# Performance work log

Measured on AMD Instinct MI355X. Metric: run time of the kernel, lower is better.

The kernel has to match this reference:

```python
import jax, jax.numpy as jnp
import numpy as np

HEAD = 16

def setup_inputs() -> dict:
    key = jax.random.key(0)
    k1, k2, k3 = jax.random.split(key, 3)
    B, S, D = 2, 2048, 1024
    x = jax.random.normal(k1, (B, S, D), dtype=jnp.float32)
    w_qkv = jax.random.normal(k2, (D, 3 * D), dtype=jnp.float32) * (1.0 / np.sqrt(D))
    b_qkv = jnp.zeros((3 * D,), dtype=jnp.float32)
    w_out = jax.random.normal(k3, (D, D), dtype=jnp.float32) * (1.0 / np.sqrt(D))
    b_out = jnp.zeros((D,), dtype=jnp.float32)
    return {"x": x, "w_qkv": w_qkv, "b_qkv": b_qkv, "w_out": w_out, "b_out": b_out}


def reference(x, w_qkv, b_qkv, w_out, b_out):
    B, S, D = x.shape
    hd = D // HEAD  # head dim
    qkv = x @ w_qkv + b_qkv                      # [B,S,3D]
    qkv = qkv.reshape(B, S, 3, HEAD, hd)
    qkv = jnp.transpose(qkv, (2, 0, 3, 1, 4))    # [3,B,H,S,hd]
    q, k, v = qkv[0], qkv[1], qkv[2]
    scores = jnp.einsum('bhqd,bhkd->bhqk', q, k)  # [B,H,S,S]
    causal = jnp.triu(jnp.ones((S, S), dtype=bool), k=1)
    scores = jnp.where(causal, -jnp.inf, scores)
    scores = scores / jnp.sqrt(jnp.asarray(hd, dtype=x.dtype))
    attn = jax.nn.softmax(scores, axis=-1)
    z = jnp.einsum('bhqk,bhkd->bhqd', attn, v)   # [B,H,S,hd]
    z = jnp.transpose(z, (0, 2, 1, 3)).reshape(B, S, D)
    out = z @ w_out + b_out
    return out
```

## Files before the change

### kernel.cpp

```cpp
#include <hip/hip_runtime.h>

#define S_LEN  2048
#define NH     16
#define HD     64
#define DMODEL 1024

using bf16x8 = __attribute__((ext_vector_type(8))) __bf16;
using f32x4  = __attribute__((ext_vector_type(4))) float;

__device__ __forceinline__ unsigned short f2bf(float f) {
    unsigned u = __float_as_uint(f);
    u += 0x7FFFu + ((u >> 16) & 1u);
    return (unsigned short)(u >> 16);
}
__device__ __forceinline__ unsigned pk_trunc(float lo, float hi) {
    return __builtin_amdgcn_perm(__float_as_uint(hi), __float_as_uint(lo), 0x07060302u);
}

#define EXP2(x) __builtin_amdgcn_exp2f(x)

#define GLDS16(gsrc, ldst) \
    __builtin_amdgcn_global_load_lds((__attribute__((address_space(1))) void*)(gsrc), \
                                     (__attribute__((address_space(3))) void*)(ldst), 16, 0, 0)

#define WAIT_LGKM0() __builtin_amdgcn_s_waitcnt(0xC07F)

#define ASM_VMCNT(n)  asm volatile("s_waitcnt vmcnt(" #n ")" ::: "memory")
#define ASM_BARRIER() asm volatile("s_barrier" ::: "memory")

__global__ __launch_bounds__(256) void prep_kernel(
    const float* __restrict__ x, const float* __restrict__ w_qkv,
    const float* __restrict__ w_out,
    unsigned short* __restrict__ xb, unsigned short* __restrict__ wqkvT,
    unsigned short* __restrict__ woutT) {
    __shared__ float T[32][33];
    int bx = blockIdx.x;
    if (bx < 4096) {
        int idx = (bx * 256 + threadIdx.x) * 4;
        float4 v = *(const float4*)(x + idx);
        ushort4 o;
        o.x = f2bf(v.x); o.y = f2bf(v.y); o.z = f2bf(v.z); o.w = f2bf(v.w);
        *(ushort4*)(xb + idx) = o;
        return;
    }
    int tb = bx - 4096;
    int tcol = tb & 127, krow = tb >> 7;
    const float* in;
    unsigned short* out;
    int N, nbx;
    if (tcol < 96) { in = w_qkv; out = wqkvT; N = 3072; nbx = tcol; }
    else           { in = w_out; out = woutT; N = 1024; nbx = tcol - 96; }
    int r  = threadIdx.x >> 3;
    int c4 = (threadIdx.x & 7) * 4;
    int kbase = krow * 32, nbase = nbx * 32;
    float4 v = *(const float4*)(in + (size_t)(kbase + r) * N + nbase + c4);
    T[r][c4 + 0] = v.x; T[r][c4 + 1] = v.y; T[r][c4 + 2] = v.z; T[r][c4 + 3] = v.w;
    __syncthreads();
    ushort4 o;
    o.x = f2bf(T[c4 + 0][r]); o.y = f2bf(T[c4 + 1][r]);
    o.z = f2bf(T[c4 + 2][r]); o.w = f2bf(T[c4 + 3][r]);
    *(ushort4*)(out + (size_t)(nbase + r) * 1024 + kbase + c4) = o;
}

template <int NI, int NT>
__device__ __forceinline__ void mfma_mainloop64(const unsigned short* __restrict__ A,
                                                const unsigned short* __restrict__ B,
                                                int m0, int n0,
                                                unsigned short* As, unsigned short* Bs,
                                                f32x4 acc[4][NI]) {
    constexpr int K = NT * 64;
    const int lane = threadIdx.x & 63, wave = threadIdx.x >> 6;
    const int quad = lane >> 4, l15 = lane & 15;
    const int wm0 = (wave >> 1) * 64, wn0 = (wave & 1) * (NI * 16);

    auto stageA = [&](int t) {
        unsigned short* Ad = As + (t % 3) * 8192;
        #pragma unroll
        for (int j = 0; j < 4; ++j) {
            int c0 = j * 256 + wave * 64;
            int c  = c0 + lane;
            int r = c >> 3, pc = c & 7, q = pc ^ (r & 7);
            GLDS16(A + (size_t)(m0 + r) * K + t * 64 + q * 8, Ad + c0 * 8);
        }
    };
    auto stageB = [&](int t) {
        unsigned short* Bd = Bs + (t & 1) * (NI * 2048);
        #pragma unroll
        for (int j = 0; j < NI; ++j) {
            int c0 = j * 256 + wave * 64;
            int c  = c0 + lane;
            int r = c >> 3, pc = c & 7, q = pc ^ (r & 7);
            GLDS16(B + (size_t)(n0 + r) * K + t * 64 + q * 8, Bd + c0 * 8);
        }
    };

    stageB(0); stageA(0);
    stageB(1); stageA(1);
    stageA(2);

    #pragma unroll
    for (int t = 0; t < NT; ++t) {
        if (t < NT - 1) { ASM_VMCNT(4); } else { ASM_VMCNT(0); }
        ASM_BARRIER();
        if (t >= 1) {
            if (t + 1 < NT) stageB(t + 1);
            if (t + 2 < NT) stageA(t + 2);
        }

        const unsigned short* Ab = As + (t % 3) * 8192;
        const unsigned short* Bb = Bs + (t & 1) * (NI * 2048);
        bf16x8 af[2][4], bfr[2][NI];
        #pragma unroll
        for (int mi = 0; mi < 4; ++mi) {
            int r = wm0 + mi * 16 + l15, x = r & 7;
            af[0][mi] = *(const bf16x8*)(Ab + r * 64 + ((quad    ) ^ x) * 8);
            af[1][mi] = *(const bf16x8*)(Ab + r * 64 + ((4 + quad) ^ x) * 8);
        }
        #pragma unroll
        for (int ni = 0; ni < NI; ++ni) {
            int r = wn0 + ni * 16 + l15, x = r & 7;
            bfr[0][ni] = *(const bf16x8*)(Bb + r * 64 + ((quad    ) ^ x) * 8);
            bfr[1][ni] = *(const bf16x8*)(Bb + r * 64 + ((4 + quad) ^ x) * 8);
        }
        #pragma unroll
        for (int h = 0; h < 2; ++h)
            #pragma unroll
            for (int mi = 0; mi < 4; ++mi)
                #pragma unroll
                for (int ni = 0; ni < NI; ++ni)
                    acc[mi][ni] = __builtin_amdgcn_mfma_f32_16x16x32_bf16(
                        af[h][mi], bfr[h][ni], acc[mi][ni], 0, 0, 0);
    }
}

__global__ __launch_bounds__(256) void gemm_qkv_kernel(
    const unsigned short* __restrict__ xb, const unsigned short* __restrict__ wT,
    const float* __restrict__ bias,
    unsigned short* __restrict__ Qt, unsigned short* __restrict__ Kh,
    unsigned short* __restrict__ Vt) {
    __shared__ __align__(16) unsigned short Sh[40960];
    unsigned short* As = Sh;
    unsigned short* Bs = Sh + 24576;

    f32x4 acc[4][4];
    #pragma unroll
    for (int i = 0; i < 4; ++i)
        #pragma unroll
        for (int j = 0; j < 4; ++j) acc[i][j] = (f32x4){0.f, 0.f, 0.f, 0.f};

    const int bid = blockIdx.x;
    const int xcd = bid & 7, slot = bid >> 3;
    const int nt = xcd * 3 + (slot % 3);
    const int mt = slot / 3;
    const int m0 = mt * 128, n0 = nt * 128;
    mfma_mainloop64<4, 16>(xb, wT, m0, n0, As, Bs, acc);

    const int lane = threadIdx.x & 63, wave = threadIdx.x >> 6;
    const int quad = lane >> 4, l15 = lane & 15;
    const int wm0 = (wave >> 1) * 64, wn0 = (wave & 1) * 64;

    const int colbase = n0 + wn0;
    const int t = colbase >> 10;
    const int h = (colbase >> 6) & (NH - 1);
    const float qscale = (t == 0) ? 0.125f * 1.44269504088896f : 1.0f;
    float bv[4];
    #pragma unroll
    for (int ni = 0; ni < 4; ++ni) bv[ni] = bias[colbase + ni * 16 + l15];

    __syncthreads();
    unsigned short* Lw = Sh + wave * 1536;

    #pragma unroll
    for (int mi = 0; mi < 4; ++mi) {
        int mbase = m0 + wm0 + mi * 16;
        int b = mbase >> 11, sbase = mbase & (S_LEN - 1);
        if (t == 1) {
            #pragma unroll
            for (int ni = 0; ni < 4; ++ni)
                #pragma unroll
                for (int r = 0; r < 4; ++r)
                    Lw[(quad * 4 + r) * 72 + ni * 16 + l15] =
                        f2bf(acc[mi][ni][r] + bv[ni]);
            WAIT_LGKM0();
            int rr = lane & 15, dc = (lane >> 4) * 16;
            uint4 v0 = *(const uint4*)(Lw + rr * 72 + dc);
            uint4 v1 = *(const uint4*)(Lw + rr * 72 + dc + 8);
            unsigned short* dst =
                Kh + ((size_t)(b * NH + h) * S_LEN + sbase + rr) * HD + dc;
            *(uint4*)dst = v0;
            *(uint4*)(dst + 8) = v1;
        } else {
            #pragma unroll
            for (int ni = 0; ni < 4; ++ni)
                #pragma unroll
                for (int r = 0; r < 4; ++r)
                    Lw[(ni * 16 + l15) * 24 + quad * 4 + r] =
                        f2bf((acc[mi][ni][r] + bv[ni]) * qscale);
            WAIT_LGKM0();
            int c = lane;
            uint4 v0 = *(const uint4*)(Lw + c * 24);
            uint4 v1 = *(const uint4*)(Lw + c * 24 + 8);
            unsigned short* base = (t == 0) ? Qt : Vt;
            unsigned short* dst =
                base + ((size_t)(b * NH + h) * HD + c) * S_LEN + sbase;
            *(uint4*)dst = v0;
            *(uint4*)(dst + 8) = v1;
        }
        WAIT_LGKM0();
    }
}

__global__ __launch_bounds__(256) void gemm_out_kernel(
    const unsigned short* __restrict__ zb, const unsigned short* __restrict__ wT,
    const float* __restrict__ bias, float* __restrict__ out) {
    __shared__ __align__(16) unsigned short As[24576], Bs[8192];
    f32x4 acc[4][2];
    #pragma unroll
    for (int i = 0; i < 4; ++i)
        #pragma unroll
        for (int j = 0; j < 2; ++j) acc[i][j] = (f32x4){0.f, 0.f, 0.f, 0.f};

    const int bid = blockIdx.x;
    const int xcd = bid & 7, slot = bid >> 3;
    const int nt = xcd * 2 + (slot & 1);
    const int mt = slot >> 1;
    const int m0 = mt * 128, n0 = nt * 64;
    mfma_mainloop64<2, 16>(zb, wT, m0, n0, As, Bs, acc);

    const int lane = threadIdx.x & 63, wave = threadIdx.x >> 6;
    const int quad = lane >> 4, l15 = lane & 15;
    const int wm0 = (wave >> 1) * 64, wn0 = (wave & 1) * 32;
    #pragma unroll
    for (int mi = 0; mi < 4; ++mi) {
        #pragma unroll
        for (int ni = 0; ni < 2; ++ni) {
            int col = n0 + wn0 + ni * 16 + l15;
            float bvv = bias[col];
            #pragma unroll
            for (int r = 0; r < 4; ++r)
                out[(size_t)(m0 + wm0 + mi * 16 + quad * 4 + r) * DMODEL + col] =
                    acc[mi][ni][r] + bvv;
        }
    }
}

__device__ const int g_sched[24 * 4] = {
    15,0,15,0,  15,16,31,1,  7,0,15,-1,
    14,0,14,0,  14,15,29,1,  6,0,13,-1,
    13,0,13,0,  13,14,27,1,
    12,0,12,0,  12,13,25,1,  5,0,11,-1,
    11,0,11,0,  11,12,23,1,
    10,0,10,0,  10,11,21,1,  4,0,9,-1,
     9,0,9,0,    9,10,19,1,
     8,0,8,0,    8,9,17,1,   3,0,7,-1,
     2,0,5,-1,   1,0,3,-1,   0,0,1,-1
};

__global__ __launch_bounds__(512) void attn_mfma_kernel(
    const unsigned short* __restrict__ Qt, const unsigned short* __restrict__ Kh,
    const unsigned short* __restrict__ Vt, unsigned short* __restrict__ zb,
    float* __restrict__ Zp, float* __restrict__ lp) {
    __shared__ __align__(16) unsigned short Ks[2 * 64 * 64];
    __shared__ __align__(16) unsigned short Vs[2 * 64 * 64];
    __shared__ __align__(16) unsigned short Pl[8 * 16 * 64];

    const int lane = threadIdx.x & 63, wave = threadIdx.x >> 6;
    const int quad = lane >> 4, l15 = lane & 15;
    const int bh = blockIdx.x;
    const int qt   = g_sched[blockIdx.y * 4 + 0];
    const int klo  = g_sched[blockIdx.y * 4 + 1];
    const int khi  = g_sched[blockIdx.y * 4 + 2];
    const int part = g_sched[blockIdx.y * 4 + 3];
    const int q0 = qt * 128;
    const float M0 = 12.0f;

    bf16x8 qf0, qf1;
    {
        const unsigned short* qb = Qt + (size_t)bh * HD * S_LEN + q0 + wave * 16 + l15;
        union { bf16x8 v; unsigned short u[8]; } u0, u1;
        #pragma unroll
        for (int j = 0; j < 8; ++j) {
            u0.u[j] = qb[(quad * 8 + j) * S_LEN];
            u1.u[j] = qb[(32 + quad * 8 + j) * S_LEN];
        }
        qf0 = u0.v; qf1 = u1.v;
    }
    bf16x8 onesv;
    {
        union { bf16x8 v; unsigned short u[8]; } uo;
        #pragma unroll
        for (int j = 0; j < 8; ++j) uo.u[j] = 0x3F80;
        onesv = uo.v;
    }

    f32x4 Z[4];
    #pragma unroll
    for (int i = 0; i < 4; ++i) Z[i] = (f32x4){0.f, 0.f, 0.f, 0.f};
    f32x4 racc = (f32x4){0.f, 0.f, 0.f, 0.f};

    unsigned short* pw = Pl + wave * 1024;
    const int pwrow = l15 * 64;

    auto stageKV = [&](int kt, int b) {
        {
            int c0 = wave * 64;
            int c  = c0 + lane;
            int r = c >> 3, pc = c & 7, q = pc ^ (r & 7);
            GLDS16(Kh + ((size_t)bh * S_LEN + kt * 64 + r) * HD + q * 8,
                   Ks + b * 4096 + c0 * 8);
        }
        {
            int c0 = wave * 64;
            int c  = c0 + lane;
            int d = c >> 3, pc = c & 7, q = pc ^ (d & 7);
            GLDS16(Vt + ((size_t)bh * HD + d) * S_LEN + kt * 64 + q * 8,
                   Vs + b * 4096 + c0 * 8);
        }
    };

    auto body = [&](int kt, int cb, bool pref) {
        if (pref) {
            stageKV(kt + 1, cb ^ 1);
            ASM_VMCNT(2);
        } else {
            ASM_VMCNT(0);
        }
        ASM_BARRIER();

        const unsigned short* Kb = Ks + cb * 4096;
        const unsigned short* Vb = Vs + cb * 4096;

        const int kq = kt - 2 * qt;
        const int dw = wave - (kq << 2);

        if (kq < 0 || dw >= 4) {
            #pragma unroll
            for (int n = 0; n < 4; ++n) {
                int woff = pwrow + (((2 * n + (quad >> 1)) ^ (l15 & 7)) << 3) + (quad & 1) * 4;
                int rk = n * 16 + l15;
                int x = rk & 7;
                bf16x8 kv0 = *(const bf16x8*)(Kb + rk * 64 + ((quad    ) ^ x) * 8);
                bf16x8 kv1 = *(const bf16x8*)(Kb + rk * 64 + ((4 + quad) ^ x) * 8);
                f32x4 t4 = (f32x4){-M0, -M0, -M0, -M0};
                __builtin_amdgcn_s_setprio(1);
                t4 = __builtin_amdgcn_mfma_f32_16x16x32_bf16(kv0, qf0, t4, 0, 0, 0);
                t4 = __builtin_amdgcn_mfma_f32_16x16x32_bf16(kv1, qf1, t4, 0, 0, 0);
                __builtin_amdgcn_s_setprio(0);
                uint2 pk;
                pk.x = pk_trunc(EXP2(t4[0]), EXP2(t4[1]));
                pk.y = pk_trunc(EXP2(t4[2]), EXP2(t4[3]));
                *(uint2*)(pw + woff) = pk;
            }
            #pragma unroll
            for (int kh = 0; kh < 2; ++kh) {
                bf16x8 pa = *(const bf16x8*)(pw + pwrow + ((kh * 4 + quad) ^ (l15 & 7)) * 8);
                __builtin_amdgcn_s_setprio(1);
                racc = __builtin_amdgcn_mfma_f32_16x16x32_bf16(onesv, pa, racc, 0, 0, 0);
                #pragma unroll
                for (int ni = 0; ni < 4; ++ni) {
                    int rd = ni * 16 + l15;
                    bf16x8 vb = *(const bf16x8*)(Vb + rd * 64 + ((kh * 4 + quad) ^ (rd & 7)) * 8);
                    Z[ni] = __builtin_amdgcn_mfma_f32_16x16x32_bf16(vb, pa, Z[ni], 0, 0, 0);
                }
                __builtin_amdgcn_s_setprio(0);
            }
        } else if (dw >= 0) {
            const int nmax = dw;
            const int qthr = dw * 16 + l15 - quad * 4;
            #pragma unroll
            for (int n = 0; n < 4; ++n) {
                int woff = pwrow + (((2 * n + (quad >> 1)) ^ (l15 & 7)) << 3) + (quad & 1) * 4;
                if (n <= nmax) {
                    int rk = n * 16 + l15;
                    int x = rk & 7;
                    bf16x8 kv0 = *(const bf16x8*)(Kb + rk * 64 + ((quad    ) ^ x) * 8);
                    bf16x8 kv1 = *(const bf16x8*)(Kb + rk * 64 + ((4 + quad) ^ x) * 8);
                    f32x4 t4 = (f32x4){-M0, -M0, -M0, -M0};
                    __builtin_amdgcn_s_setprio(1);
                    t4 = __builtin_amdgcn_mfma_f32_16x16x32_bf16(kv0, qf0, t4, 0, 0, 0);
                    t4 = __builtin_amdgcn_mfma_f32_16x16x32_bf16(kv1, qf1, t4, 0, 0, 0);
                    __builtin_amdgcn_s_setprio(0);
                    float p[4];
                    #pragma unroll
                    for (int r = 0; r < 4; ++r) {
                        p[r] = EXP2(t4[r]);
                        if ((n * 16 + r) > qthr) p[r] = 0.f;
                    }
                    uint2 pk;
                    pk.x = pk_trunc(p[0], p[1]);
                    pk.y = pk_trunc(p[2], p[3]);
                    *(uint2*)(pw + woff) = pk;
                } else {
                    *(uint2*)(pw + woff) = (uint2){0u, 0u};
                }
            }
            const int khmax = dw >> 1;
            for (int kh = 0; kh <= khmax; ++kh) {
                bf16x8 pa = *(const bf16x8*)(pw + pwrow + ((kh * 4 + quad) ^ (l15 & 7)) * 8);
                __builtin_amdgcn_s_setprio(1);
                racc = __builtin_amdgcn_mfma_f32_16x16x32_bf16(onesv, pa, racc, 0, 0, 0);
                #pragma unroll
                for (int ni = 0; ni < 4; ++ni) {
                    int rd = ni * 16 + l15;
                    bf16x8 vb = *(const bf16x8*)(Vb + rd * 64 + ((kh * 4 + quad) ^ (rd & 7)) * 8);
                    Z[ni] = __builtin_amdgcn_mfma_f32_16x16x32_bf16(vb, pa, Z[ni], 0, 0, 0);
                }
                __builtin_amdgcn_s_setprio(0);
            }
        }
        ASM_BARRIER();
    };

    stageKV(klo, 0);
    {
        int cnt = khi - klo + 1;
        int kt = klo;
        while (cnt >= 2) {
            body(kt, 0, true);
            body(kt + 1, 1, cnt > 2);
            kt += 2; cnt -= 2;
        }
        if (cnt == 1) body(kt, 0, false);
    }

    const float rsum = racc[0];

    const int ql = wave * 16 + l15;
    if (part < 0) {
        const int b = bh >> 4, h = bh & (NH - 1);
        float inv = 1.f / rsum;
        size_t rowoff = (size_t)(b * S_LEN + q0 + ql) * DMODEL + h * HD;
        #pragma unroll
        for (int ni = 0; ni < 4; ++ni) {
            ushort4 o;
            o.x = f2bf(Z[ni][0] * inv);
            o.y = f2bf(Z[ni][1] * inv);
            o.z = f2bf(Z[ni][2] * inv);
            o.w = f2bf(Z[ni][3] * inv);
            *(ushort4*)(zb + rowoff + ni * 16 + quad * 4) = o;
        }
    } else {
        const int slot = (qt - 8) * 2 + part;
        float* zpo = Zp + ((size_t)(slot * 32 + bh) * 128 + ql) * 64;
        #pragma unroll
        for (int ni = 0; ni < 4; ++ni) {
            float4 st;
            st.x = Z[ni][0]; st.y = Z[ni][1]; st.z = Z[ni][2]; st.w = Z[ni][3];
            *(float4*)(zpo + ni * 16 + quad * 4) = st;
        }
        if (quad == 0)
            lp[(size_t)(slot * 32 + bh) * 128 + ql] = rsum;
    }
}

__global__ __launch_bounds__(256) void attn_merge_kernel(
    const float* __restrict__ Zp, const float* __restrict__ lp,
    unsigned short* __restrict__ zb) {
    const int bh = blockIdx.x, qi = blockIdx.y, qt = 8 + qi;
    const int t = threadIdx.x;
    const int q = t >> 1;
    const int d0 = (t & 1) << 5;
    const int s0 = qi * 2, s1 = s0 + 1;
    float l = lp[(size_t)(s0 * 32 + bh) * 128 + q] +
              lp[(size_t)(s1 * 32 + bh) * 128 + q];
    float inv = 1.f / l;
    const float* z0 = Zp + ((size_t)(s0 * 32 + bh) * 128 + q) * 64 + d0;
    const float* z1 = Zp + ((size_t)(s1 * 32 + bh) * 128 + q) * 64 + d0;
    const int b = bh >> 4, h = bh & (NH - 1);
    unsigned short* o =
        zb + (size_t)(b * S_LEN + qt * 128 + q) * DMODEL + h * HD + d0;
    #pragma unroll
    for (int i = 0; i < 32; i += 4) {
        float4 a = *(const float4*)(z0 + i);
        float4 c = *(const float4*)(z1 + i);
        ushort4 ov;
        ov.x = f2bf((a.x + c.x) * inv);
        ov.y = f2bf((a.y + c.y) * inv);
        ov.z = f2bf((a.z + c.z) * inv);
        ov.w = f2bf((a.w + c.w) * inv);
        *(ushort4*)(o + i) = ov;
    }
}

extern "C" void kernel_launch(void* const* d_in, const int* in_sizes, int n_in,
                              void* d_out, int out_size, void* d_ws, size_t ws_size,
                              hipStream_t stream)
{
    const float* x     = (const float*)d_in[0];
    const float* w_qkv = (const float*)d_in[1];
    const float* b_qkv = (const float*)d_in[2];
    const float* w_out = (const float*)d_in[3];
    const float* b_out = (const float*)d_in[4];
    float* out = (float*)d_out;

    unsigned short* wsu   = (unsigned short*)d_ws;
    unsigned short* xb    = wsu;
    unsigned short* wqkvT = xb    + (size_t)4194304;
    unsigned short* woutT = wqkvT + (size_t)3145728;
    unsigned short* Qt    = woutT + (size_t)1048576;
    unsigned short* Kh    = Qt    + (size_t)4194304;
    unsigned short* Vt    = Kh    + (size_t)4194304;
    unsigned short* zb    = Vt    + (size_t)4194304;
    float* Zp = (float*)(zb + (size_t)4194304);
    float* lp = Zp + (size_t)16 * 32 * 128 * 64;

    prep_kernel<<<dim3(8192), 256, 0, stream>>>(x, w_qkv, w_out, xb, wqkvT, woutT);

    gemm_qkv_kernel<<<dim3(768), 256, 0, stream>>>(
        xb, wqkvT, b_qkv, Qt, Kh, Vt);

    attn_mfma_kernel<<<dim3(2 * NH, 24), 512, 0, stream>>>(Qt, Kh, Vt, zb, Zp, lp);
    attn_merge_kernel<<<dim3(2 * NH, 8), 256, 0, stream>>>(Zp, lp, zb);

    gemm_out_kernel<<<dim3(512), 256, 0, stream>>>(
        zb, woutT, b_out, out);
}
```

Measured before the change: 169.9 us.

## Double attention query tile to 256 rows with 16 waves and rebalanced split schedule

Grows each attention block from 8 to 16 waves so it covers 256 query rows, which halves how often K/V tiles are staged per query. K and V staging now go to separate wave groups, each issuing one load. The split-KV schedule is rebuilt into 15 work items with 2–3 partitions per long query tile, and the merge kernel is generalized to sum a variable number of partials. The risks are larger blocks (1024 threads, more LDS for P) cutting occupancy, and a coarser schedule with fewer blocks for tail balance.

```diff
diff --git a/kernel.cpp b/kernel.cpp
--- a/kernel.cpp
+++ b/kernel.cpp
@@ -244,25 +244,21 @@
     }
 }
 
-__device__ const int g_sched[24 * 4] = {
-    15,0,15,0,  15,16,31,1,  7,0,15,-1,
-    14,0,14,0,  14,15,29,1,  6,0,13,-1,
-    13,0,13,0,  13,14,27,1,
-    12,0,12,0,  12,13,25,1,  5,0,11,-1,
-    11,0,11,0,  11,12,23,1,
-    10,0,10,0,  10,11,21,1,  4,0,9,-1,
-     9,0,9,0,    9,10,19,1,
-     8,0,8,0,    8,9,17,1,   3,0,7,-1,
-     2,0,5,-1,   1,0,3,-1,   0,0,1,-1
+__device__ const int g_sched[15 * 4] = {
+    5,0,11,6,   5,12,23,7,  2,0,11,-1,
+    7,0,10,0,   7,11,21,1,  7,22,31,2,
+    6,0,9,3,    4,0,9,8,    4,10,19,9,
+    6,10,18,4,  6,19,27,5,
+    3,0,7,10,   3,8,15,11,  1,0,7,-1,  0,0,3,-1
 };
 
-__global__ __launch_bounds__(512) void attn_mfma_kernel(
+__global__ __launch_bounds__(1024, 8) void attn_mfma_kernel(
     const unsigned short* __restrict__ Qt, const unsigned short* __restrict__ Kh,
     const unsigned short* __restrict__ Vt, unsigned short* __restrict__ zb,
     float* __restrict__ Zp, float* __restrict__ lp) {
     __shared__ __align__(16) unsigned short Ks[2 * 64 * 64];
     __shared__ __align__(16) unsigned short Vs[2 * 64 * 64];
-    __shared__ __align__(16) unsigned short Pl[8 * 16 * 64];
+    __shared__ __align__(16) unsigned short Pl[16 * 16 * 64];
 
     const int lane = threadIdx.x & 63, wave = threadIdx.x >> 6;
     const int quad = lane >> 4, l15 = lane & 15;
@@ -271,7 +267,7 @@
     const int klo  = g_sched[blockIdx.y * 4 + 1];
     const int khi  = g_sched[blockIdx.y * 4 + 2];
     const int part = g_sched[blockIdx.y * 4 + 3];
-    const int q0 = qt * 128;
+    const int q0 = qt * 256;
     const float M0 = 12.0f;
 
     bf16x8 qf0, qf1;
@@ -302,15 +298,14 @@
     const int pwrow = l15 * 64;
 
     auto stageKV = [&](int kt, int b) {
-        {
+        if (wave < 8) {
             int c0 = wave * 64;
             int c  = c0 + lane;
             int r = c >> 3, pc = c & 7, q = pc ^ (r & 7);
             GLDS16(Kh + ((size_t)bh * S_LEN + kt * 64 + r) * HD + q * 8,
                    Ks + b * 4096 + c0 * 8);
-        }
-        {
-            int c0 = wave * 64;
+        } else {
+            int c0 = (wave - 8) * 64;
             int c  = c0 + lane;
             int d = c >> 3, pc = c & 7, q = pc ^ (d & 7);
             GLDS16(Vt + ((size_t)bh * HD + d) * S_LEN + kt * 64 + q * 8,
@@ -321,7 +316,7 @@
     auto body = [&](int kt, int cb, bool pref) {
         if (pref) {
             stageKV(kt + 1, cb ^ 1);
-            ASM_VMCNT(2);
+            ASM_VMCNT(1);
         } else {
             ASM_VMCNT(0);
         }
@@ -330,7 +325,7 @@
         const unsigned short* Kb = Ks + cb * 4096;
         const unsigned short* Vb = Vs + cb * 4096;
 
-        const int kq = kt - 2 * qt;
+        const int kq = kt - 4 * qt;
         const int dw = wave - (kq << 2);
 
         if (kq < 0 || dw >= 4) {
@@ -440,8 +435,7 @@
             *(ushort4*)(zb + rowoff + ni * 16 + quad * 4) = o;
         }
     } else {
-        const int slot = (qt - 8) * 2 + part;
-        float* zpo = Zp + ((size_t)(slot * 32 + bh) * 128 + ql) * 64;
+        float* zpo = Zp + ((size_t)(part * 32 + bh) * 256 + ql) * 64;
         #pragma unroll
         for (int ni = 0; ni < 4; ++ni) {
             float4 st;
@@ -449,36 +443,45 @@
             *(float4*)(zpo + ni * 16 + quad * 4) = st;
         }
         if (quad == 0)
-            lp[(size_t)(slot * 32 + bh) * 128 + ql] = rsum;
+            lp[(size_t)(part * 32 + bh) * 256 + ql] = rsum;
     }
 }
 
 __global__ __launch_bounds__(256) void attn_merge_kernel(
     const float* __restrict__ Zp, const float* __restrict__ lp,
     unsigned short* __restrict__ zb) {
-    const int bh = blockIdx.x, qi = blockIdx.y, qt = 8 + qi;
+    const int qt_tab[5] = {7, 6, 5, 4, 3};
+    const int s0_tab[5] = {0, 3, 6, 8, 10};
+    const int np_tab[5] = {3, 3, 2, 2, 2};
+    const int bh = blockIdx.x, y = blockIdx.y;
+    const int qt = qt_tab[y], s0 = s0_tab[y], np = np_tab[y];
     const int t = threadIdx.x;
-    const int q = t >> 1;
-    const int d0 = (t & 1) << 5;
-    const int s0 = qi * 2, s1 = s0 + 1;
-    float l = lp[(size_t)(s0 * 32 + bh) * 128 + q] +
-              lp[(size_t)(s1 * 32 + bh) * 128 + q];
-    float inv = 1.f / l;
-    const float* z0 = Zp + ((size_t)(s0 * 32 + bh) * 128 + q) * 64 + d0;
-    const float* z1 = Zp + ((size_t)(s1 * 32 + bh) * 128 + q) * 64 + d0;
     const int b = bh >> 4, h = bh & (NH - 1);
-    unsigned short* o =
-        zb + (size_t)(b * S_LEN + qt * 128 + q) * DMODEL + h * HD + d0;
-    #pragma unroll
-    for (int i = 0; i < 32; i += 4) {
-        float4 a = *(const float4*)(z0 + i);
-        float4 c = *(const float4*)(z1 + i);
-        ushort4 ov;
-        ov.x = f2bf((a.x + c.x) * inv);
-        ov.y = f2bf((a.y + c.y) * inv);
-        ov.z = f2bf((a.z + c.z) * inv);
-        ov.w = f2bf((a.w + c.w) * inv);
-        *(ushort4*)(o + i) = ov;
+    #pragma unroll
+    for (int chunk = 0; chunk < 4; ++chunk) {
+        const int q  = chunk * 64 + (t >> 2);
+        const int d0 = (t & 3) << 4;
+        float l = 0.f;
+        for (int p = 0; p < np; ++p)
+            l += lp[(size_t)((s0 + p) * 32 + bh) * 256 + q];
+        float inv = 1.f / l;
+        unsigned short* o =
+            zb + (size_t)(b * S_LEN + qt * 256 + q) * DMODEL + h * HD + d0;
+        #pragma unroll
+        for (int i = 0; i < 16; i += 4) {
+            float4 s = {0.f, 0.f, 0.f, 0.f};
+            for (int p = 0; p < np; ++p) {
+                const float* zp = Zp + ((size_t)((s0 + p) * 32 + bh) * 256 + q) * 64 + d0 + i;
+                float4 a = *(const float4*)zp;
+                s.x += a.x; s.y += a.y; s.z += a.z; s.w += a.w;
+            }
+            ushort4 ov;
+            ov.x = f2bf(s.x * inv);
+            ov.y = f2bf(s.y * inv);
+            ov.z = f2bf(s.z * inv);
+            ov.w = f2bf(s.w * inv);
+            *(ushort4*)(o + i) = ov;
+        }
     }
 }
 
@@ -502,15 +505,15 @@
     unsigned short* Vt    = Kh    + (size_t)4194304;
     unsigned short* zb    = Vt    + (size_t)4194304;
     float* Zp = (float*)(zb + (size_t)4194304);
-    float* lp = Zp + (size_t)16 * 32 * 128 * 64;
+    float* lp = Zp + (size_t)12 * 32 * 256 * 64;
 
     prep_kernel<<<dim3(8192), 256, 0, stream>>>(x, w_qkv, w_out, xb, wqkvT, woutT);
 
     gemm_qkv_kernel<<<dim3(768), 256, 0, stream>>>(
         xb, wqkvT, b_qkv, Qt, Kh, Vt);
 
-    attn_mfma_kernel<<<dim3(2 * NH, 24), 512, 0, stream>>>(Qt, Kh, Vt, zb, Zp, lp);
-    attn_merge_kernel<<<dim3(2 * NH, 8), 256, 0, stream>>>(Zp, lp, zb);
+    attn_mfma_kernel<<<dim3(2 * NH, 15), 1024, 0, stream>>>(Qt, Kh, Vt, zb, Zp, lp);
+    attn_merge_kernel<<<dim3(2 * NH, 5), 256, 0, stream>>>(Zp, lp, zb);
 
     gemm_out_kernel<<<dim3(512), 256, 0, stream>>>(
         zb, woutT, b_out, out);
```

Result: slower. 193.2 us (+13.8%).
